# Optimization experiments

Measured on AMD Instinct MI355X. Metric: run time of the kernel, lower is better.

The kernel has to match this reference:

```python
import jax, jax.numpy as jnp
import numpy as np

N_SRC, N_DST, K, T = 16384, 8192, 16, 2
NODE_IN, EDGE_IN, TIME_D = 128, 64, 128
D_MODEL = NODE_IN + TIME_D + EDGE_IN  # 320
N_HEAD, D_K = 8, 64                   # d_k = d_v
HID = 128
LN_EPS = 1e-5


def setup_inputs() -> dict:
    key = jax.random.key(0)
    ks = jax.random.split(key, 10)
    std_qk = np.sqrt(2.0 / (D_MODEL + D_K)).astype(np.float32)
    return {
        "node_features": jax.random.normal(ks[0], (N_SRC, NODE_IN), jnp.float32),
        "edge_features": jax.random.normal(ks[1], (N_DST, K, T, EDGE_IN), jnp.float32),
        "delta_t": jax.random.uniform(ks[2], (N_DST, K, T), jnp.float32) * 100.0,
        "neigh_idx": jax.random.randint(ks[3], (N_DST, K), 0, N_SRC),
        "basis_freq": jnp.asarray(1.0 / 10 ** np.linspace(0, 9, TIME_D), jnp.float32),
        "phase": jnp.zeros((TIME_D,), jnp.float32),
        "w_qs": jax.random.normal(ks[4], (N_HEAD * D_K, D_MODEL), jnp.float32) * std_qk,
        "w_ks": jax.random.normal(ks[5], (N_HEAD * D_K, D_MODEL), jnp.float32) * std_qk,
        "w_vs": jax.random.normal(ks[6], (N_HEAD * D_K, D_MODEL), jnp.float32) * std_qk,
        "fc_w": jax.random.normal(ks[7], (D_MODEL, N_HEAD * D_K), jnp.float32) * 0.03,
        "fc_b": jnp.zeros((D_MODEL,), jnp.float32),
        "ln_g": jnp.ones((D_MODEL,), jnp.float32),
        "ln_b": jnp.zeros((D_MODEL,), jnp.float32),
        "node_w": jax.random.normal(ks[8], (HID, 2 * NODE_IN + TIME_D + EDGE_IN), jnp.float32) * 0.05,
        "node_b": jnp.zeros((HID,), jnp.float32),
    }


def reference(node_features, edge_features, delta_t, neigh_idx, basis_freq, phase,
              w_qs, w_ks, w_vs, fc_w, fc_b, ln_g, ln_b, node_w, node_b):
    h_dst = node_features[:N_DST]                                  # [N, NODE_IN]
    # message_func: per-edge time encoding + gather src feats + concat
    te = jnp.cos(delta_t[..., None] * basis_freq + phase)          # [N, K, T, TIME_D]
    h_nb = node_features[neigh_idx]                                # [N, K, NODE_IN] (irregular gather)
    h_nb = jnp.broadcast_to(h_nb[:, :, None, :], (N_DST, K, T, NODE_IN))
    m = jnp.concatenate([h_nb, edge_features, te], axis=-1)        # [N, K, T, D_MODEL]
    m = m.reshape(N_DST, K * T, D_MODEL)                           # mailbox kv
    # reduce_func query: [h_dst, zeros(edge_in), time_encode(0)=cos(phase)]
    t0 = jnp.broadcast_to(jnp.cos(phase), (N_DST, TIME_D))
    q = jnp.concatenate([h_dst, jnp.zeros((N_DST, EDGE_IN), h_dst.dtype), t0], axis=-1)  # [N, D_MODEL]
    # multi-head attention (len_q = 1)
    qh = (q @ w_qs.T).reshape(N_DST, N_HEAD, D_K)
    kh = (m @ w_ks.T).reshape(N_DST, K * T, N_HEAD, D_K)
    vh = (m @ w_vs.T).reshape(N_DST, K * T, N_HEAD, D_K)
    scores = jnp.einsum('nhd,nlhd->nhl', qh, kh) / np.float32(np.sqrt(D_K))
    attn = jax.nn.softmax(scores, axis=-1)
    ctx = jnp.einsum('nhl,nlhd->nhd', attn, vh).reshape(N_DST, N_HEAD * D_K)
    out = ctx @ fc_w.T + fc_b
    x = out + q                                                    # residual
    mu = x.mean(-1, keepdims=True)
    var = x.var(-1, keepdims=True)
    h_neigh = ln_g * (x - mu) * jax.lax.rsqrt(var + LN_EPS) + ln_b  # layer norm
    h = jnp.concatenate([h_dst, h_neigh], axis=-1)                 # [N, 2*NODE_IN+TIME_D+EDGE_IN]
    return jax.nn.relu(h @ node_w.T + node_b)                      # [N, HID]
```

## Files before the change

kernel.cpp:

```cpp
#include <hip/hip_runtime.h>
#include <math.h>

#define LNB      32
#define NODE_IN  128
#define EDGE_IN  64
#define TIME_D   128
#define D_MODEL  320
#define N_HEAD   8
#define D_K      64
#define NHD      512
#define HID      128
#define IN2      448
#define N_DSTN   8192

typedef __attribute__((ext_vector_type(8))) short bf16x8;
typedef __attribute__((ext_vector_type(4))) float f32x4;
#define MFMA16(a,b,c) __builtin_amdgcn_mfma_f32_16x16x32_bf16(a,b,c,0,0,0)

#define WS_QKM   0
#define WS_WQK   20971520
#define WS_WVF   21299200
#define WS_NWC   22118400
#define WS_F32   22175744
#define WS_X     22182784

#define F_C0     0
#define F_C0K    512
#define F_CC     3072
#define F_B2     3392

__device__ __forceinline__ unsigned short f2bf(float f) {
  __bf16 h = (__bf16)f;
  return __builtin_bit_cast(unsigned short, h);
}
__device__ __forceinline__ bf16x8 pack8(const float* v) {
  unsigned short b8[8];
  #pragma unroll
  for (int j = 0; j < 8; ++j) b8[j] = f2bf(v[j]);
  return *(const bf16x8*)b8;
}

__global__ __launch_bounds__(256)
void prep1a(const float* __restrict__ nw, const float* __restrict__ lng,
            const float* __restrict__ fcb, const float* __restrict__ ph,
            unsigned short* __restrict__ ws)
{
  int i = blockIdx.x * 256 + threadIdx.x;
  unsigned short* nwc = ws + WS_NWC;
  float* f32r = (float*)(ws + WS_F32);
  if (i < 16384) {
    int o = i >> 7, k = i & 127;
    nwc[o * IN2 + k] = f2bf(nw[(size_t)o * IN2 + k]);
  } else if (i < 57344) {
    int j = i - 16384, o = j / 320, c = j - o * 320;
    nwc[o * IN2 + 128 + c] = f2bf(nw[(size_t)o * IN2 + 128 + c] * lng[c]);
  } else if (i < 57664) {
    int c = i - 57344;
    f32r[F_CC + c] = fcb[c] + (c >= 192 ? __cosf(ph[c - 192]) : 0.f);
  }
}

__global__ __launch_bounds__(256)
void prep1b(const float* __restrict__ wq, const float* __restrict__ ph,
            const float* __restrict__ nw, const float* __restrict__ lnb_,
            const float* __restrict__ nb, unsigned short* __restrict__ ws)
{
  float* f32r = (float*)(ws + WS_F32);
  int gw = (blockIdx.x * 256 + threadIdx.x) >> 6;
  int ln = threadIdx.x & 63;
  if (gw < 512) {
    float s = __cosf(ph[ln])      * wq[(size_t)gw * D_MODEL + 192 + ln]
            + __cosf(ph[ln + 64]) * wq[(size_t)gw * D_MODEL + 256 + ln];
    #pragma unroll
    for (int off = 32; off >= 1; off >>= 1) s += __shfl_xor(s, off);
    if (ln == 0) f32r[F_C0 + gw] = s;
  } else {
    int o = gw - 512;
    float s = 0.f;
    #pragma unroll
    for (int k = 0; k < 5; ++k) {
      int c = ln + 64 * k;
      s += nw[(size_t)o * IN2 + 128 + c] * lnb_[c];
    }
    #pragma unroll
    for (int off = 32; off >= 1; off >>= 1) s += __shfl_xor(s, off);
    if (ln == 0) f32r[F_B2 + o] = nb[o] + s;
  }
}

__global__ __launch_bounds__(256)
void prep_c0k(const float* __restrict__ wk, unsigned short* __restrict__ ws)
{
  float* f32r = (float*)(ws + WS_F32);
  int gw = (blockIdx.x * 256 + threadIdx.x) >> 6;
  int ln = threadIdx.x & 63;
  int h = gw / 320, d = gw - h * 320;
  float s = f32r[F_C0 + h * 64 + ln] * wk[(size_t)(h * 64 + ln) * D_MODEL + d];
  #pragma unroll
  for (int off = 32; off >= 1; off >>= 1) s += __shfl_xor(s, off);
  if (ln == 0) f32r[F_C0K + gw] = s;
}

__global__ __launch_bounds__(256)
void prep_wqk(const float* __restrict__ wq, const float* __restrict__ wk,
              unsigned short* __restrict__ ws)
{
  __shared__ float sQw[64 * 128];
  __shared__ float sKw[64 * 32];
  int h = blockIdx.x / 10, d0 = (blockIdx.x - h * 10) * 32;
  int tid = threadIdx.x;
  #pragma unroll 4
  for (int it = 0; it < 32; ++it) {
    int idx = it * 256 + tid;
    int r = idx >> 7, c = idx & 127;
    sQw[idx] = wq[(size_t)(h * 64 + r) * D_MODEL + c];
  }
  #pragma unroll
  for (int it = 0; it < 8; ++it) {
    int idx = it * 256 + tid;
    int r = idx >> 5, c = idx & 31;
    sKw[idx] = wk[(size_t)(h * 64 + r) * D_MODEL + d0 + c];
  }
  __syncthreads();
  int di = tid >> 3, k0 = (tid & 7) * 16;
  float acc[16] = {};
  for (int dk = 0; dk < 64; ++dk) {
    float w = sKw[dk * 32 + di];
    #pragma unroll
    for (int j = 0; j < 16; ++j) acc[j] += w * sQw[dk * 128 + k0 + j];
  }
  unsigned short* dst = ws + WS_WQK + (size_t)(h * 320 + d0 + di) * 128 + k0;
  #pragma unroll
  for (int j = 0; j < 16; ++j) dst[j] = f2bf(acc[j]);
}

__global__ __launch_bounds__(256)
void prep_wvf(const float* __restrict__ fcw, const float* __restrict__ wv,
              unsigned short* __restrict__ ws)
{
  __shared__ float sF[32 * 64];
  __shared__ float sW[64 * 32];
  int b = blockIdx.x;
  int h = b / 100, r2 = b - h * 100;
  int ct = r2 / 10;
  int c0 = ct * 32, d0 = (r2 - ct * 10) * 32;
  int tid = threadIdx.x;
  #pragma unroll
  for (int it = 0; it < 8; ++it) {
    int idx = it * 256 + tid;
    int i = idx >> 6, jj = idx & 63;
    sF[idx] = fcw[(size_t)(c0 + i) * NHD + h * 64 + jj];
  }
  #pragma unroll
  for (int it = 0; it < 8; ++it) {
    int idx = it * 256 + tid;
    int jj = idx >> 5, i = idx & 31;
    sW[idx] = wv[(size_t)(h * 64 + jj) * D_MODEL + d0 + i];
  }
  __syncthreads();
  int ci = tid >> 3, dj0 = (tid & 7) * 4;
  float acc[4] = {};
  for (int jj = 0; jj < 64; ++jj) {
    float f = sF[ci * 64 + jj];
    #pragma unroll
    for (int k = 0; k < 4; ++k) acc[k] += f * sW[jj * 32 + dj0 + k];
  }
  unsigned short* wvf = ws + WS_WVF;
  #pragma unroll
  for (int k = 0; k < 4; ++k)
    wvf[(size_t)(c0 + ci) * 2560 + (size_t)(d0 + dj0 + k) * 8 + h] = f2bf(acc[k]);
}

__global__ __launch_bounds__(256, 6)
void tgat_qk(const float* __restrict__ nf, const unsigned short* __restrict__ ws,
             unsigned short* __restrict__ qkm)
{
  __shared__ alignas(16) unsigned short sA[64 * 136];
  const int tid = threadIdx.x, wid = tid >> 6, lane = tid & 63, qd = lane >> 4, lm = lane & 15;
  const int mt_blk = blockIdx.x / 20, nt_blk = blockIdx.x - mt_blk * 20;
  const int n0 = mt_blk * 64, c0 = nt_blk * 128;
  const unsigned short* wqk = ws + WS_WQK;
  const float* f32r = (const float*)(ws + WS_F32);

  {
    int n = tid >> 2, k0 = (tid & 3) * 32;
    const float4* src = (const float4*)(nf + (size_t)(n0 + n) * NODE_IN + k0);
    #pragma unroll
    for (int q = 0; q < 4; ++q) {
      float4 f0 = src[2 * q], f1 = src[2 * q + 1];
      float v[8] = {f0.x, f0.y, f0.z, f0.w, f1.x, f1.y, f1.z, f1.w};
      *(bf16x8*)&sA[n * 136 + k0 + q * 8] = pack8(v);
    }
  }
  __syncthreads();

  f32x4 acc[2][4] = {};
  for (int kt = 0; kt < 4; ++kt) {
    bf16x8 a[4];
    #pragma unroll
    for (int mt = 0; mt < 4; ++mt)
      a[mt] = *(const bf16x8*)&sA[(mt * 16 + lm) * 136 + kt * 32 + qd * 8];
    #pragma unroll
    for (int t = 0; t < 2; ++t) {
      int cg = c0 + (2 * wid + t) * 16 + lm;
      bf16x8 b = *(const bf16x8*)&wqk[(size_t)cg * 128 + kt * 32 + qd * 8];
      #pragma unroll
      for (int mt = 0; mt < 4; ++mt) acc[t][mt] = MFMA16(a[mt], b, acc[t][mt]);
    }
  }
  #pragma unroll
  for (int t = 0; t < 2; ++t) {
    int cg = c0 + (2 * wid + t) * 16 + lm;
    float ck = f32r[F_C0K + cg];
    #pragma unroll
    for (int mt = 0; mt < 4; ++mt)
      #pragma unroll
      for (int r = 0; r < 4; ++r)
        qkm[(size_t)(n0 + mt * 16 + qd * 4 + r) * 2560 + cg] = f2bf(acc[t][mt][r] + ck);
  }
}

__global__ __launch_bounds__(256, 6)
void tgat_attn(const float* __restrict__ nf, const float* __restrict__ ef,
               const float* __restrict__ dtp, const int* __restrict__ nidx,
               const float* __restrict__ freq, const float* __restrict__ ph,
               unsigned short* __restrict__ qkm)
{
  __shared__ alignas(16) unsigned short sM[LNB * 328];
  __shared__ alignas(16) unsigned short sATT[16 * 40];

  const int tid = threadIdx.x;
  const int wid = tid >> 6, lane = tid & 63, qd = lane >> 4, lm = lane & 15;
  const int n = blockIdx.x;
  unsigned short* qn = qkm + (size_t)n * 2560;

  #pragma unroll 1
  for (int it = 0; it < 5; ++it) {
    int g = it * 256 + tid;
    int l = g & 31, dg = g >> 5;
    int d0 = dg * 8;
    float v[8];
    if (dg < 16) {
      int ni = nidx[n * 16 + (l >> 1)];
      const float4* src = (const float4*)(nf + (size_t)ni * NODE_IN + d0);
      float4 f0 = src[0], f1 = src[1];
      v[0]=f0.x; v[1]=f0.y; v[2]=f0.z; v[3]=f0.w; v[4]=f1.x; v[5]=f1.y; v[6]=f1.z; v[7]=f1.w;
    } else if (dg < 24) {
      const float4* src = (const float4*)(ef + ((size_t)n * LNB + l) * EDGE_IN + (d0 - NODE_IN));
      float4 f0 = src[0], f1 = src[1];
      v[0]=f0.x; v[1]=f0.y; v[2]=f0.z; v[3]=f0.w; v[4]=f1.x; v[5]=f1.y; v[6]=f1.z; v[7]=f1.w;
    } else {
      int dd = d0 - 192;
      float dt = dtp[(size_t)n * LNB + l];
      const float4* fq = (const float4*)(freq + dd);
      const float4* pp = (const float4*)(ph + dd);
      float4 q0 = fq[0], q1 = fq[1], p0 = pp[0], p1 = pp[1];
      v[0] = __cosf(dt * q0.x + p0.x); v[1] = __cosf(dt * q0.y + p0.y);
      v[2] = __cosf(dt * q0.z + p0.z); v[3] = __cosf(dt * q0.w + p0.w);
      v[4] = __cosf(dt * q1.x + p1.x); v[5] = __cosf(dt * q1.y + p1.y);
      v[6] = __cosf(dt * q1.z + p1.z); v[7] = __cosf(dt * q1.w + p1.w);
    }
    *(bf16x8*)&sM[l * 328 + d0] = pack8(v);
  }

  bf16x8 qfrag[10];
  if (wid == 0) {
    #pragma unroll
    for (int kt = 0; kt < 10; ++kt) {
      qfrag[kt] = (bf16x8){0,0,0,0,0,0,0,0};
      if (lm < 8) qfrag[kt] = *(const bf16x8*)&qn[lm * 320 + kt * 32 + qd * 8];
    }
  }
  __syncthreads();

  const int tbeg = (wid == 0) ? 0 : 2 + (wid - 1) * 6;
  const int tcnt = (wid == 0) ? 2 : 6;
  bf16x8 afr[6];

  if (wid == 0) {
    f32x4 acc0 = {}, acc1 = {};
    #pragma unroll
    for (int kt = 0; kt < 10; ++kt) {
      bf16x8 a0 = *(const bf16x8*)&sM[lm * 328 + kt * 32 + qd * 8];
      bf16x8 a1 = *(const bf16x8*)&sM[(16 + lm) * 328 + kt * 32 + qd * 8];
      acc0 = MFMA16(a0, qfrag[kt], acc0);
      acc1 = MFMA16(a1, qfrag[kt], acc1);
    }
    float s[8], e[8];
    #pragma unroll
    for (int r = 0; r < 4; ++r) { s[r] = acc0[r] * 0.125f; s[4 + r] = acc1[r] * 0.125f; }
    float mx = s[0];
    #pragma unroll
    for (int i = 1; i < 8; ++i) mx = fmaxf(mx, s[i]);
    mx = fmaxf(mx, __shfl_xor(mx, 16));
    mx = fmaxf(mx, __shfl_xor(mx, 32));
    float sum = 0.f;
    #pragma unroll
    for (int i = 0; i < 8; ++i) { e[i] = __expf(s[i] - mx); sum += e[i]; }
    sum += __shfl_xor(sum, 16);
    sum += __shfl_xor(sum, 32);
    float inv = 1.f / sum;
    #pragma unroll
    for (int i = 0; i < 8; ++i) {
      int l = (i < 4) ? (qd * 4 + i) : (16 + qd * 4 + (i - 4));
      sATT[lm * 40 + l] = f2bf(e[i] * inv);
    }
  } else {
    #pragma unroll
    for (int u = 0; u < 6; ++u) {
      int d = (tbeg + u) * 16 + lm;
      unsigned short a8[8];
      #pragma unroll
      for (int j = 0; j < 8; ++j) a8[j] = sM[(qd * 8 + j) * 328 + d];
      afr[u] = *(const bf16x8*)a8;
    }
  }
  __syncthreads();

  if (wid == 0) {
    #pragma unroll
    for (int u = 0; u < 2; ++u) {
      int d = u * 16 + lm;
      unsigned short a8[8];
      #pragma unroll
      for (int j = 0; j < 8; ++j) a8[j] = sM[(qd * 8 + j) * 328 + d];
      afr[u] = *(const bf16x8*)a8;
    }
  }
  bf16x8 batt = *(const bf16x8*)&sATT[lm * 40 + qd * 8];
  #pragma unroll
  for (int u = 0; u < 6; ++u) {
    if (u < tcnt) {
      int dtile = tbeg + u;
      f32x4 acc = {};
      acc = MFMA16(afr[u], batt, acc);
      if (lm < 8) {
        #pragma unroll
        for (int r = 0; r < 4; ++r)
          qn[(dtile * 16 + qd * 4 + r) * 8 + lm] = f2bf(acc[r]);
      }
    }
  }
}

__global__ __launch_bounds__(512, 2)
void tgat_xgemm(const unsigned short* __restrict__ ws,
                const unsigned short* __restrict__ qkm, float* __restrict__ xacc)
{
  __shared__ float sRed[32 * 324];
  const int tid = threadIdx.x, wid = tid >> 6, lane = tid & 63;
  const int qd = lane >> 4, lm = lane & 15;
  const int kh = wid >> 2, cs = wid & 3;
  const int n0 = blockIdx.x * 32;
  const unsigned short* wvf = ws + WS_WVF;

  const unsigned short* A0 = qkm + (size_t)(n0 + lm) * 2560 + kh * 1280 + qd * 8;
  const unsigned short* A1 = A0 + (size_t)16 * 2560;
  const unsigned short* B0 = wvf + (size_t)(cs * 80 + lm) * 2560 + kh * 1280 + qd * 8;

  f32x4 acc[2][5] = {};
  #pragma unroll 4
  for (int kt = 0; kt < 40; ++kt) {
    bf16x8 a0 = *(const bf16x8*)(A0 + kt * 32);
    bf16x8 a1 = *(const bf16x8*)(A1 + kt * 32);
    #pragma unroll
    for (int u = 0; u < 5; ++u) {
      bf16x8 b = *(const bf16x8*)(B0 + (size_t)u * 16 * 2560 + kt * 32);
      acc[0][u] = MFMA16(a0, b, acc[0][u]);
      acc[1][u] = MFMA16(a1, b, acc[1][u]);
    }
  }

  if (kh == 1) {
    #pragma unroll
    for (int mt = 0; mt < 2; ++mt)
      #pragma unroll
      for (int u = 0; u < 5; ++u)
        #pragma unroll
        for (int r = 0; r < 4; ++r)
          sRed[(mt * 16 + qd * 4 + r) * 324 + cs * 80 + u * 16 + lm] = acc[mt][u][r];
  }
  __syncthreads();
  if (kh == 0) {
    #pragma unroll
    for (int mt = 0; mt < 2; ++mt)
      #pragma unroll
      for (int u = 0; u < 5; ++u)
        #pragma unroll
        for (int r = 0; r < 4; ++r) {
          int row = mt * 16 + qd * 4 + r, col = cs * 80 + u * 16 + lm;
          xacc[(size_t)(n0 + row) * 320 + col] = acc[mt][u][r] + sRed[row * 324 + col];
        }
  }
}

__global__ __launch_bounds__(256, 4)
void tgat_post2(const float* __restrict__ nf, const unsigned short* __restrict__ ws,
                const float* __restrict__ xacc, float* __restrict__ out)
{
  __shared__ alignas(16) unsigned short sQb[16 * 136];
  __shared__ alignas(16) unsigned short sXb[16 * 328];
  const int tid = threadIdx.x, wid = tid >> 6, lane = tid & 63, qd = lane >> 4, lm = lane & 15;
  const int n0 = blockIdx.x * 16;
  const unsigned short* nwc = ws + WS_NWC;
  const float* f32r = (const float*)(ws + WS_F32);

  {
    int nn = tid >> 4, kk = (tid & 15) * 8;
    const float4* src = (const float4*)(nf + (size_t)(n0 + nn) * NODE_IN + kk);
    float4 f0 = src[0], f1 = src[1];
    float v8[8] = {f0.x, f0.y, f0.z, f0.w, f1.x, f1.y, f1.z, f1.w};
    *(bf16x8*)&sQb[nn * 136 + kk] = pack8(v8);
  }
  const int rr = tid >> 4, cl = tid & 15;
  float v[20], s1 = 0.f, s2 = 0.f;
  #pragma unroll
  for (int u = 0; u < 20; ++u) {
    int c = u * 16 + cl;
    float x = xacc[(size_t)(n0 + rr) * 320 + c] + f32r[F_CC + c];
    if (c < 128) x += nf[(size_t)(n0 + rr) * NODE_IN + c];
    v[u] = x; s1 += x; s2 += x * x;
  }
  #pragma unroll
  for (int off = 8; off >= 1; off >>= 1) { s1 += __shfl_xor(s1, off); s2 += __shfl_xor(s2, off); }
  float mean = s1 * (1.f / D_MODEL);
  float var  = s2 * (1.f / D_MODEL) - mean * mean;
  float rstd = rsqrtf(var + 1e-5f);
  #pragma unroll
  for (int u = 0; u < 20; ++u) {
    int c = u * 16 + cl;
    sXb[rr * 328 + c] = f2bf((v[u] - mean) * rstd);
  }
  __syncthreads();

  #pragma unroll
  for (int t = 0; t < 2; ++t) {
    int o = (wid * 2 + t) * 16 + lm;
    f32x4 acc = {};
    for (int kt = 0; kt < 14; ++kt) {
      bf16x8 a;
      if (kt < 4) a = *(const bf16x8*)&sQb[lm * 136 + kt * 32 + qd * 8];
      else        a = *(const bf16x8*)&sXb[lm * 328 + (kt - 4) * 32 + qd * 8];
      bf16x8 b = *(const bf16x8*)&nwc[(size_t)o * IN2 + kt * 32 + qd * 8];
      acc = MFMA16(a, b, acc);
    }
    float bz = f32r[F_B2 + o];
    #pragma unroll
    for (int r = 0; r < 4; ++r)
      out[(size_t)(n0 + qd * 4 + r) * HID + o] = fmaxf(acc[r] + bz, 0.f);
  }
}

extern "C" void kernel_launch(void* const* d_in, const int* in_sizes, int n_in,
                              void* d_out, int out_size, void* d_ws, size_t ws_size,
                              hipStream_t stream) {
  const float* nf   = (const float*)d_in[0];
  const float* ef   = (const float*)d_in[1];
  const float* dtp  = (const float*)d_in[2];
  const int*   nidx = (const int*)  d_in[3];
  const float* freq = (const float*)d_in[4];
  const float* ph   = (const float*)d_in[5];
  const float* wq   = (const float*)d_in[6];
  const float* wk   = (const float*)d_in[7];
  const float* wv   = (const float*)d_in[8];
  const float* fcw  = (const float*)d_in[9];
  const float* fcb  = (const float*)d_in[10];
  const float* lng  = (const float*)d_in[11];
  const float* lnb_ = (const float*)d_in[12];
  const float* nw   = (const float*)d_in[13];
  const float* nb   = (const float*)d_in[14];
  float* out = (float*)d_out;
  unsigned short* ws = (unsigned short*)d_ws;
  unsigned short* qkm = ws + WS_QKM;
  float* xacc = (float*)(ws + WS_X);

  prep1a  <<<226, 256, 0, stream>>>(nw, lng, fcb, ph, ws);
  prep1b  <<<160, 256, 0, stream>>>(wq, ph, nw, lnb_, nb, ws);
  prep_c0k<<<640, 256, 0, stream>>>(wk, ws);
  prep_wqk<<<80,  256, 0, stream>>>(wq, wk, ws);
  prep_wvf<<<800, 256, 0, stream>>>(fcw, wv, ws);
  tgat_qk   <<<2560, 256, 0, stream>>>(nf, ws, qkm);
  tgat_attn <<<8192, 256, 0, stream>>>(nf, ef, dtp, nidx, freq, ph, qkm);
  tgat_xgemm<<<256,  512, 0, stream>>>(ws, qkm, xacc);
  tgat_post2<<<512,  256, 0, stream>>>(nf, ws, xacc, out);
}
```

Baseline: 285.8 us.

## Fuse xgemm with layernorm/output GEMM and stage A tiles through swizzled LDS

Merges the post-processing kernel (residual, layer norm, final node GEMM with ReLU) into the xgemm kernel, so the fp32 x accumulator no longer round-trips through global memory. The A operand is now double-buffered through LDS with an XOR swizzle, and B fragments are register-prefetched two k-steps ahead. The cost is much larger LDS use, occupancy lowered to one block per CU, and only 256 blocks doing the post stage instead of 512.

```diff
diff --git a/kernel.cpp b/kernel.cpp
--- a/kernel.cpp
+++ b/kernel.cpp
@@ -22,7 +22,6 @@
 #define WS_WVF   21299200
 #define WS_NWC   22118400
 #define WS_F32   22175744
-#define WS_X     22182784
 
 #define F_C0     0
 #define F_C0K    512
@@ -343,68 +342,102 @@
   }
 }
 
-__global__ __launch_bounds__(512, 2)
-void tgat_xgemm(const unsigned short* __restrict__ ws,
-                const unsigned short* __restrict__ qkm, float* __restrict__ xacc)
-{
-  __shared__ float sRed[32 * 324];
+__global__ __launch_bounds__(512, 1)
+void tgat_xgemm(const float* __restrict__ nf, const unsigned short* __restrict__ ws,
+                const unsigned short* __restrict__ qkm, float* __restrict__ out)
+{
+  __shared__ alignas(16) unsigned short sAb[2 * 20480];
+  __shared__ alignas(16) unsigned short sXb[32 * 328];
+  __shared__ alignas(16) unsigned short sQb[32 * 136];
   const int tid = threadIdx.x, wid = tid >> 6, lane = tid & 63;
   const int qd = lane >> 4, lm = lane & 15;
   const int kh = wid >> 2, cs = wid & 3;
   const int n0 = blockIdx.x * 32;
   const unsigned short* wvf = ws + WS_WVF;
-
-  const unsigned short* A0 = qkm + (size_t)(n0 + lm) * 2560 + kh * 1280 + qd * 8;
-  const unsigned short* A1 = A0 + (size_t)16 * 2560;
-  const unsigned short* B0 = wvf + (size_t)(cs * 80 + lm) * 2560 + kh * 1280 + qd * 8;
+  const unsigned short* nwc = ws + WS_NWC;
+  const float* f32r = (const float*)(ws + WS_F32);
+
+  bf16x8 st[5];
+  #define STAGE_LOAD(p) {                                                      \
+    _Pragma("unroll")                                                          \
+    for (int i = 0; i < 5; ++i) {                                              \
+      int o = i * 8192 + tid * 16;                                             \
+      int kh2 = o / 20480, o2 = o - kh2 * 20480;                               \
+      int r = o2 / 640, b = o2 - r * 640;                                      \
+      st[i] = *(const bf16x8*)(qkm + (size_t)(n0 + r) * 2560 + kh2 * 1280      \
+                               + (p) * 320 + (b >> 1));                        \
+    } }
+  #define STAGE_WRITE(q) {                                                     \
+    unsigned short* dst = sAb + (q) * 20480;                                   \
+    _Pragma("unroll")                                                          \
+    for (int i = 0; i < 5; ++i) {                                              \
+      int o = i * 8192 + tid * 16;                                             \
+      int kh2 = o / 20480, o2 = o - kh2 * 20480;                               \
+      int r = o2 / 640, b = o2 - r * 640;                                      \
+      *(bf16x8*)&dst[kh2 * 10240 + r * 320 + ((b ^ ((r & 7) << 4)) >> 1)] = st[i]; \
+    } }
 
   f32x4 acc[2][5] = {};
-  #pragma unroll 4
-  for (int kt = 0; kt < 40; ++kt) {
-    bf16x8 a0 = *(const bf16x8*)(A0 + kt * 32);
-    bf16x8 a1 = *(const bf16x8*)(A1 + kt * 32);
-    #pragma unroll
-    for (int u = 0; u < 5; ++u) {
-      bf16x8 b = *(const bf16x8*)(B0 + (size_t)u * 16 * 2560 + kt * 32);
-      acc[0][u] = MFMA16(a0, b, acc[0][u]);
-      acc[1][u] = MFMA16(a1, b, acc[1][u]);
-    }
-  }
-
-  if (kh == 1) {
+  const unsigned short* Bcol = wvf + (size_t)(cs * 80 + lm) * 2560 + kh * 1280 + qd * 8;
+
+  STAGE_LOAD(0); STAGE_WRITE(0);
+  __syncthreads();
+
+  for (int p = 0; p < 4; ++p) {
+    if (p < 3) STAGE_LOAD(p + 1);
+    const unsigned short* Ab = sAb + (p & 1) * 20480 + kh * 10240;
+    const unsigned short* Bp = Bcol + p * 320;
+    bf16x8 breg[3][5];
+    #pragma unroll
+    for (int s = 0; s < 2; ++s)
+      #pragma unroll
+      for (int u = 0; u < 5; ++u)
+        breg[s][u] = *(const bf16x8*)(Bp + (size_t)u * 16 * 2560 + s * 32);
+    #pragma unroll
+    for (int kt = 0; kt < 10; ++kt) {
+      const int cur = kt % 3, nxt = (kt + 2) % 3;
+      if (kt + 2 < 10) {
+        #pragma unroll
+        for (int u = 0; u < 5; ++u)
+          breg[nxt][u] = *(const bf16x8*)(Bp + (size_t)u * 16 * 2560 + (kt + 2) * 32);
+      }
+      const int b0 = kt * 64 + qd * 16;
+      const int r0 = lm, r1 = 16 + lm;
+      bf16x8 a0 = *(const bf16x8*)&Ab[r0 * 320 + ((b0 ^ ((r0 & 7) << 4)) >> 1)];
+      bf16x8 a1 = *(const bf16x8*)&Ab[r1 * 320 + ((b0 ^ ((r1 & 7) << 4)) >> 1)];
+      #pragma unroll
+      for (int u = 0; u < 5; ++u) {
+        acc[0][u] = MFMA16(a0, breg[cur][u], acc[0][u]);
+        acc[1][u] = MFMA16(a1, breg[cur][u], acc[1][u]);
+      }
+    }
+    if (p < 3) {
+      STAGE_WRITE((p + 1) & 1);
+      __syncthreads();
+    }
+  }
+
+  __syncthreads();
+  float* sX = (float*)sAb;
+  if (kh == 0) {
     #pragma unroll
     for (int mt = 0; mt < 2; ++mt)
       #pragma unroll
       for (int u = 0; u < 5; ++u)
         #pragma unroll
         for (int r = 0; r < 4; ++r)
-          sRed[(mt * 16 + qd * 4 + r) * 324 + cs * 80 + u * 16 + lm] = acc[mt][u][r];
-  }
-  __syncthreads();
-  if (kh == 0) {
+          sX[(mt * 16 + qd * 4 + r) * 324 + cs * 80 + u * 16 + lm] = acc[mt][u][r];
+  }
+  __syncthreads();
+  if (kh == 1) {
     #pragma unroll
     for (int mt = 0; mt < 2; ++mt)
       #pragma unroll
       for (int u = 0; u < 5; ++u)
         #pragma unroll
-        for (int r = 0; r < 4; ++r) {
-          int row = mt * 16 + qd * 4 + r, col = cs * 80 + u * 16 + lm;
-          xacc[(size_t)(n0 + row) * 320 + col] = acc[mt][u][r] + sRed[row * 324 + col];
-        }
-  }
-}
-
-__global__ __launch_bounds__(256, 4)
-void tgat_post2(const float* __restrict__ nf, const unsigned short* __restrict__ ws,
-                const float* __restrict__ xacc, float* __restrict__ out)
-{
-  __shared__ alignas(16) unsigned short sQb[16 * 136];
-  __shared__ alignas(16) unsigned short sXb[16 * 328];
-  const int tid = threadIdx.x, wid = tid >> 6, lane = tid & 63, qd = lane >> 4, lm = lane & 15;
-  const int n0 = blockIdx.x * 16;
-  const unsigned short* nwc = ws + WS_NWC;
-  const float* f32r = (const float*)(ws + WS_F32);
-
+        for (int r = 0; r < 4; ++r)
+          sX[(mt * 16 + qd * 4 + r) * 324 + cs * 80 + u * 16 + lm] += acc[mt][u][r];
+  }
   {
     int nn = tid >> 4, kk = (tid & 15) * 8;
     const float4* src = (const float4*)(nf + (size_t)(n0 + nn) * NODE_IN + kk);
@@ -412,12 +445,14 @@
     float v8[8] = {f0.x, f0.y, f0.z, f0.w, f1.x, f1.y, f1.z, f1.w};
     *(bf16x8*)&sQb[nn * 136 + kk] = pack8(v8);
   }
+  __syncthreads();
+
   const int rr = tid >> 4, cl = tid & 15;
   float v[20], s1 = 0.f, s2 = 0.f;
   #pragma unroll
   for (int u = 0; u < 20; ++u) {
     int c = u * 16 + cl;
-    float x = xacc[(size_t)(n0 + rr) * 320 + c] + f32r[F_CC + c];
+    float x = sX[rr * 324 + c] + f32r[F_CC + c];
     if (c < 128) x += nf[(size_t)(n0 + rr) * NODE_IN + c];
     v[u] = x; s1 += x; s2 += x * x;
   }
@@ -435,20 +470,24 @@
 
   #pragma unroll
   for (int t = 0; t < 2; ++t) {
-    int o = (wid * 2 + t) * 16 + lm;
-    f32x4 acc = {};
+    int task = wid * 2 + t;
+    int rh = task >> 3, ot = task & 7;
+    int o = ot * 16 + lm;
+    f32x4 oacc = {};
     for (int kt = 0; kt < 14; ++kt) {
       bf16x8 a;
-      if (kt < 4) a = *(const bf16x8*)&sQb[lm * 136 + kt * 32 + qd * 8];
-      else        a = *(const bf16x8*)&sXb[lm * 328 + (kt - 4) * 32 + qd * 8];
+      if (kt < 4) a = *(const bf16x8*)&sQb[(rh * 16 + lm) * 136 + kt * 32 + qd * 8];
+      else        a = *(const bf16x8*)&sXb[(rh * 16 + lm) * 328 + (kt - 4) * 32 + qd * 8];
       bf16x8 b = *(const bf16x8*)&nwc[(size_t)o * IN2 + kt * 32 + qd * 8];
-      acc = MFMA16(a, b, acc);
+      oacc = MFMA16(a, b, oacc);
     }
     float bz = f32r[F_B2 + o];
     #pragma unroll
     for (int r = 0; r < 4; ++r)
-      out[(size_t)(n0 + qd * 4 + r) * HID + o] = fmaxf(acc[r] + bz, 0.f);
-  }
+      out[(size_t)(n0 + rh * 16 + qd * 4 + r) * HID + o] = fmaxf(oacc[r] + bz, 0.f);
+  }
+  #undef STAGE_LOAD
+  #undef STAGE_WRITE
 }
 
 extern "C" void kernel_launch(void* const* d_in, const int* in_sizes, int n_in,
@@ -472,7 +511,6 @@
   float* out = (float*)d_out;
   unsigned short* ws = (unsigned short*)d_ws;
   unsigned short* qkm = ws + WS_QKM;
-  float* xacc = (float*)(ws + WS_X);
 
   prep1a  <<<226, 256, 0, stream>>>(nw, lng, fcb, ph, ws);
   prep1b  <<<160, 256, 0, stream>>>(wq, ph, nw, lnb_, nb, ws);
@@ -481,6 +519,5 @@
   prep_wvf<<<800, 256, 0, stream>>>(fcw, wv, ws);
   tgat_qk   <<<2560, 256, 0, stream>>>(nf, ws, qkm);
   tgat_attn <<<8192, 256, 0, stream>>>(nf, ef, dtp, nidx, freq, ph, qkm);
-  tgat_xgemm<<<256,  512, 0, stream>>>(ws, qkm, xacc);
-  tgat_post2<<<512,  256, 0, stream>>>(nf, ws, xacc, out);
-}
+  tgat_xgemm<<<256,  512, 0, stream>>>(nf, ws, qkm, out);
+}
```

After: 270.3 us. -5.4%, faster.

## Tile xgemm through double-buffered LDS with direct global-to-LDS loads

Applied to the files above, without the earlier changes.

Rewrites the xgemm kernel so each block computes a 128x80 output tile. A and B chunks are staged into swizzled, double-buffered LDS using global_load_lds, where before every wave streamed its operands straight from global memory with a split-K reduction through shared memory. Blocks are remapped across XCDs so neighbouring tiles share the cache. This is meant to cut redundant global traffic and drop the split-K reduction. In exchange it lowers occupancy to one block per CU, uses a large LDS footprint, and each wave now carries only 5 accumulators.

```diff
diff --git a/kernel.cpp b/kernel.cpp
--- a/kernel.cpp
+++ b/kernel.cpp
@@ -39,6 +39,10 @@
   for (int j = 0; j < 8; ++j) b8[j] = f2bf(v[j]);
   return *(const bf16x8*)b8;
 }
+
+#define GLDS(srcp, dstp) __builtin_amdgcn_global_load_lds(                     \
+    (const __attribute__((address_space(1))) unsigned int*)(const void*)(srcp),\
+    (__attribute__((address_space(3))) unsigned int*)(void*)(dstp), 16, 0, 0)
 
 __global__ __launch_bounds__(256)
 void prep1a(const float* __restrict__ nw, const float* __restrict__ lng,
@@ -343,55 +347,65 @@
   }
 }
 
-__global__ __launch_bounds__(512, 2)
+__global__ __launch_bounds__(512, 1)
 void tgat_xgemm(const unsigned short* __restrict__ ws,
                 const unsigned short* __restrict__ qkm, float* __restrict__ xacc)
 {
-  __shared__ float sRed[32 * 324];
+  __shared__ alignas(16) unsigned short sA[2][128 * 128];
+  __shared__ alignas(16) unsigned short sB[2][80 * 128];
   const int tid = threadIdx.x, wid = tid >> 6, lane = tid & 63;
   const int qd = lane >> 4, lm = lane & 15;
-  const int kh = wid >> 2, cs = wid & 3;
-  const int n0 = blockIdx.x * 32;
+  const int xcd = blockIdx.x & 7, j = blockIdx.x >> 3;
+  const int nb = j & 3, mb = xcd + 8 * (j >> 2);
+  const int n0 = mb * 128, c0 = nb * 80;
   const unsigned short* wvf = ws + WS_WVF;
 
-  const unsigned short* A0 = qkm + (size_t)(n0 + lm) * 2560 + kh * 1280 + qd * 8;
-  const unsigned short* A1 = A0 + (size_t)16 * 2560;
-  const unsigned short* B0 = wvf + (size_t)(cs * 80 + lm) * 2560 + kh * 1280 + qd * 8;
-
-  f32x4 acc[2][5] = {};
-  #pragma unroll 4
-  for (int kt = 0; kt < 40; ++kt) {
-    bf16x8 a0 = *(const bf16x8*)(A0 + kt * 32);
-    bf16x8 a1 = *(const bf16x8*)(A1 + kt * 32);
-    #pragma unroll
-    for (int u = 0; u < 5; ++u) {
-      bf16x8 b = *(const bf16x8*)(B0 + (size_t)u * 16 * 2560 + kt * 32);
-      acc[0][u] = MFMA16(a0, b, acc[0][u]);
-      acc[1][u] = MFMA16(a1, b, acc[1][u]);
-    }
-  }
-
-  if (kh == 1) {
-    #pragma unroll
-    for (int mt = 0; mt < 2; ++mt)
+  const int rhi = lane >> 4, blo = lane & 15;
+
+  #define STAGE(kc, buf) {                                                     \
+    for (int ri = wid; ri < 52; ri += 8) {                                     \
+      if (ri < 32) {                                                           \
+        int r = ri * 4 + rhi;                                                  \
+        int blk = blo ^ (r & 7);                                               \
+        GLDS(qkm + (size_t)(n0 + r) * 2560 + (kc) * 128 + blk * 8,             \
+             &sA[buf][ri * 512]);                                              \
+      } else {                                                                 \
+        int jb = ri - 32;                                                      \
+        int r = jb * 4 + rhi;                                                  \
+        int blk = blo ^ (r & 7);                                               \
+        GLDS(wvf + (size_t)(c0 + r) * 2560 + (kc) * 128 + blk * 8,             \
+             &sB[buf][jb * 512]);                                              \
+      }                                                                        \
+    } }
+
+  f32x4 acc[5] = {};
+  STAGE(0, 0);
+  __syncthreads();
+
+  for (int c = 0; c < 20; ++c) {
+    if (c < 19) STAGE(c + 1, (c + 1) & 1);
+    const unsigned short* Ab = sA[c & 1];
+    const unsigned short* Bb = sB[c & 1];
+    const int s = lm & 7;
+    #pragma unroll
+    for (int kt = 0; kt < 4; ++kt) {
+      const int blk = ((kt << 2) | qd) ^ s;
+      bf16x8 a = *(const bf16x8*)&Ab[(wid * 16 + lm) * 128 + blk * 8];
       #pragma unroll
-      for (int u = 0; u < 5; ++u)
-        #pragma unroll
-        for (int r = 0; r < 4; ++r)
-          sRed[(mt * 16 + qd * 4 + r) * 324 + cs * 80 + u * 16 + lm] = acc[mt][u][r];
-  }
-  __syncthreads();
-  if (kh == 0) {
-    #pragma unroll
-    for (int mt = 0; mt < 2; ++mt)
-      #pragma unroll
-      for (int u = 0; u < 5; ++u)
-        #pragma unroll
-        for (int r = 0; r < 4; ++r) {
-          int row = mt * 16 + qd * 4 + r, col = cs * 80 + u * 16 + lm;
-          xacc[(size_t)(n0 + row) * 320 + col] = acc[mt][u][r] + sRed[row * 324 + col];
-        }
-  }
+      for (int u = 0; u < 5; ++u) {
+        bf16x8 b = *(const bf16x8*)&Bb[(u * 16 + lm) * 128 + blk * 8];
+        acc[u] = MFMA16(a, b, acc[u]);
+      }
+    }
+    __syncthreads();
+  }
+
+  #pragma unroll
+  for (int u = 0; u < 5; ++u)
+    #pragma unroll
+    for (int r = 0; r < 4; ++r)
+      xacc[(size_t)(n0 + wid * 16 + qd * 4 + r) * 320 + c0 + u * 16 + lm] = acc[u][r];
+  #undef STAGE
 }
 
 __global__ __launch_bounds__(256, 4)
```

New measurement: 253.8 us. 1.13x faster.
